# Optimization experiments

Hardware: AMD Instinct MI355X
Metric: run time of the kernel (lower is better)

The kernel has to match this reference:

```python
import jax, jax.numpy as jnp
import numpy as np

B, S, IN_F, OUT_F = 4, 2048, 4096, 4096
ALPHA = 0.01

def setup_inputs() -> dict:
    key = jax.random.key(0)
    k1, k2 = jax.random.split(key, 2)
    # int8-valued activations and weights (stored as int32 per harness dtype)
    x = jax.random.randint(k1, (B, S, IN_F), -127, 127, dtype=jnp.int32)
    weight = jax.random.randint(k2, (IN_F, OUT_F), -127, 127, dtype=jnp.int32)
    bias = jnp.zeros((1, OUT_F), dtype=jnp.float16)
    alpha = jnp.full((1,), ALPHA, dtype=jnp.float32)
    return {"x": x, "weight": weight, "bias": bias, "alpha": alpha}

def reference(x, weight, bias, alpha):
    # Faithful to forward's default (non-hybrid) path:
    # y = F.linear(x.float(), weight.t().float(), bias.float()) * alpha
    # F.linear(x, W^T) == x @ W, with W shape (in_features, out_features).
    x_shape = x.shape
    xf = x.reshape(-1, x_shape[-1]).astype(jnp.float32)          # [B*S, in]
    wf = weight.astype(jnp.float32)                               # [in, out]
    y = (xf @ wf + bias.astype(jnp.float32)) * alpha              # [B*S, out]
    return y.reshape(*x_shape[:-1], -1)                           # [B, S, out]
```

## Files before the change

### kernel.cpp

```cpp
#include <hip/hip_runtime.h>
#include <hip/hip_fp16.h>

using i32x4  = __attribute__((ext_vector_type(4)))  int;
using i32x16 = __attribute__((ext_vector_type(16))) int;

static constexpr int M  = 4 * 2048;
static constexpr int N  = 4096;
static constexpr int K  = 4096;
static constexpr int BM = 128, BN = 128, BK = 64;
static constexpr int NT = K / BK;
static constexpr int TILE = BM * BK;

static constexpr int PX_BLOCKS = (int)((size_t)M * K / 16 / 256);
static constexpr int PW_BLOCKS = (int)((size_t)N * K / 16 / 256);

__device__ __forceinline__ unsigned pack4(i32x4 v) {
  return (unsigned)((v.x & 255) | ((v.y & 255) << 8) | ((v.z & 255) << 16) | (v.w << 24));
}

__global__ __launch_bounds__(256) void pack_kernel(const int* __restrict__ x,
                                                   const int* __restrict__ w,
                                                   unsigned char* __restrict__ wa,
                                                   unsigned char* __restrict__ wb) {
  if (blockIdx.x < PX_BLOCKS) {
    unsigned g = blockIdx.x * 256 + threadIdx.x;
    unsigned tile = g >> 9, gt = g & 511;
    unsigned kg = gt >> 7, row = gt & 127;
    unsigned br = tile >> 6, kt = tile & 63;
    const int* src = x + ((size_t)(br * 128 + row) * K + kt * 64 + kg * 16);
    i32x4 v0 = *(const i32x4*)(src + 0);
    i32x4 v1 = *(const i32x4*)(src + 4);
    i32x4 v2 = *(const i32x4*)(src + 8);
    i32x4 v3 = *(const i32x4*)(src + 12);
    i32x4 d;
    d.x = (int)pack4(v0); d.y = (int)pack4(v1); d.z = (int)pack4(v2); d.w = (int)pack4(v3);
    *(i32x4*)(wa + (size_t)g * 16) = d;
  } else {
    unsigned g = (blockIdx.x - PX_BLOCKS) * 256 + threadIdx.x;
    unsigned tile = g >> 9, gt = g & 511;
    unsigned kg = gt >> 7, col = gt & 127;
    unsigned bn = tile >> 6, kt = tile & 63;
    unsigned n  = bn * 128 + col;
    unsigned k0 = kt * 64 + kg * 16;
    const int* src = w + (size_t)k0 * N + n;
    i32x4 d;
#pragma unroll
    for (int j = 0; j < 4; ++j) {
      int b0 = src[(size_t)(j * 4 + 0) * N];
      int b1 = src[(size_t)(j * 4 + 1) * N];
      int b2 = src[(size_t)(j * 4 + 2) * N];
      int b3 = src[(size_t)(j * 4 + 3) * N];
      d[j] = (b0 & 255) | ((b1 & 255) << 8) | ((b2 & 255) << 16) | (b3 << 24);
    }
    *(i32x4*)(wb + (size_t)g * 16) = d;
  }
}


__global__ __launch_bounds__(256) void gemm_i8(const unsigned char* __restrict__ wa,
                                               const unsigned char* __restrict__ wb,
                                               const __half* __restrict__ bias,
                                               const float* __restrict__ alphaP,
                                               float* __restrict__ out) {
  __shared__ __align__(16) unsigned char As[2][TILE];

  const int tid  = threadIdx.x;
  const int lane = tid & 63;
  const int w    = tid >> 6;
  const int wr   = w >> 1, wc = w & 1;
  const int l31  = lane & 31;
  const int kgl  = lane >> 5;

  const int bc = blockIdx.x;
  const int br = blockIdx.y;

  const unsigned char* ga = wa + (size_t)br * NT * TILE;
  const unsigned char* gb = wb + (size_t)bc * NT * TILE;

  const int arow = wr * 64 + l31;
  const int bcol = wc * 64 + l31;

  i32x4 p0, p1, q0, q1;
  i32x4 b[2][2][2];

#define GLOADA_P(T) do {                                             \
    const i32x4* ap = (const i32x4*)(ga + (size_t)(T) * TILE);       \
    p0 = ap[tid]; p1 = ap[tid + 256];                                \
  } while (0)

#define GLOADA_Q(T) do {                                             \
    const i32x4* ap = (const i32x4*)(ga + (size_t)(T) * TILE);       \
    q0 = ap[tid]; q1 = ap[tid + 256];                                \
  } while (0)

#define SWRITE_P(BUF) do {                                           \
    i32x4* aw = (i32x4*)&As[BUF][0];                                 \
    aw[tid] = p0; aw[tid + 256] = p1;                                \
  } while (0)

#define SWRITE_Q(BUF) do {                                           \
    i32x4* aw = (i32x4*)&As[BUF][0];                                 \
    aw[tid] = q0; aw[tid + 256] = q1;                                \
  } while (0)

#define BLOAD(PAR, T) do {                                           \
    const unsigned char* bt = gb + (size_t)(T) * TILE;               \
    b[PAR][0][0] = *(const i32x4*)(bt + (kgl    ) * 2048 + (bcol +  0) * 16); \
    b[PAR][0][1] = *(const i32x4*)(bt + (kgl    ) * 2048 + (bcol + 32) * 16); \
    b[PAR][1][0] = *(const i32x4*)(bt + (kgl + 2) * 2048 + (bcol +  0) * 16); \
    b[PAR][1][1] = *(const i32x4*)(bt + (kgl + 2) * 2048 + (bcol + 32) * 16); \
  } while (0)

  i32x16 acc[2][2] = {};

#define COMPUTE(BUF, PAR) do {                                                 \
    const unsigned char* Ab = &As[BUF][0] + kgl * 2048;                        \
    _Pragma("unroll")                                                          \
    for (int kc = 0; kc < 2; ++kc) {                                           \
      const unsigned char* Ap = Ab + kc * 4096;                                \
      i32x4 a0 = *(const i32x4*)(Ap + (arow +  0) * 16);                       \
      i32x4 a1 = *(const i32x4*)(Ap + (arow + 32) * 16);                       \
      acc[0][0] = __builtin_amdgcn_mfma_i32_32x32x32_i8(a0, b[PAR][kc][0], acc[0][0], 0, 0, 0); \
      acc[0][1] = __builtin_amdgcn_mfma_i32_32x32x32_i8(a0, b[PAR][kc][1], acc[0][1], 0, 0, 0); \
      acc[1][0] = __builtin_amdgcn_mfma_i32_32x32x32_i8(a1, b[PAR][kc][0], acc[1][0], 0, 0, 0); \
      acc[1][1] = __builtin_amdgcn_mfma_i32_32x32x32_i8(a1, b[PAR][kc][1], acc[1][1], 0, 0, 0); \
    }                                                                          \
  } while (0)

  GLOADA_P(0);
  BLOAD(0, 0);
  SWRITE_P(0);
  GLOADA_Q(1);
  BLOAD(1, 1);
  __syncthreads();

  for (int t = 0; t < NT; t += 2) {
    if (t + 2 < NT) GLOADA_P(t + 2);
    COMPUTE(0, 0);
    if (t + 2 < NT) BLOAD(0, t + 2);
    __builtin_amdgcn_sched_barrier(0);
    if (t + 1 < NT) SWRITE_Q(1);
    __syncthreads();

    if (t + 3 < NT) GLOADA_Q(t + 3);
    COMPUTE(1, 1);
    if (t + 3 < NT) BLOAD(1, t + 3);
    __builtin_amdgcn_sched_barrier(0);
    if (t + 2 < NT) SWRITE_P(0);
    __syncthreads();
  }

  const float alpha = *alphaP;
  const int row0 = br * 128 + wr * 64 + 4 * kgl;
  const int col0 = bc * 128 + wc * 64 + l31;
#pragma unroll
  for (int ni = 0; ni < 2; ++ni) {
    const int col = col0 + ni * 32;
    const float bf = __half2float(bias[col]);
#pragma unroll
    for (int mi = 0; mi < 2; ++mi) {
#pragma unroll
      for (int r = 0; r < 16; ++r) {
        const int row = row0 + mi * 32 + (r & 3) + 8 * (r >> 2);
        out[(size_t)row * N + col] = ((float)acc[mi][ni][r] + bf) * alpha;
      }
    }
  }
#undef COMPUTE
#undef GLOADA_P
#undef GLOADA_Q
#undef SWRITE_P
#undef SWRITE_Q
#undef BLOAD
}

extern "C" void kernel_launch(void* const* d_in, const int* in_sizes, int n_in,
                              void* d_out, int out_size, void* d_ws, size_t ws_size,
                              hipStream_t stream) {
  const int*    x     = (const int*)d_in[0];
  const int*    wgt   = (const int*)d_in[1];
  const __half* bias  = (const __half*)d_in[2];
  const float*  alpha = (const float*)d_in[3];
  float*        out   = (float*)d_out;

  unsigned char* wa = (unsigned char*)d_ws;
  unsigned char* wb = wa + (size_t)M * K;

  pack_kernel<<<PX_BLOCKS + PW_BLOCKS, 256, 0, stream>>>(x, wgt, wa, wb);

  dim3 grid(N / BN, M / BM);
  gemm_i8<<<grid, 256, 0, stream>>>(wa, wb, bias, alpha, out);
}
```

Baseline: 224.8 us.

## Enlarge GEMM tiles to 256x256 with 512 threads and swizzled block order

Block tiles grow from 128x128 to 256x256 with 8 waves per block, each wave computing 64x128 (2x4 MFMA accumulators). The pack layout is changed to match, the grid becomes 1D with a swizzled block-to-tile mapping, and B is prefetched directly from global memory into registers one tile ahead. The aim is higher arithmetic intensity per loaded byte and better L2 locality. In exchange, each wave uses more accumulator registers and each block needs 32KB of LDS, which may lower occupancy.

```diff
diff --git a/kernel.cpp b/kernel.cpp
--- a/kernel.cpp
+++ b/kernel.cpp
@@ -7,9 +7,10 @@
 static constexpr int M  = 4 * 2048;
 static constexpr int N  = 4096;
 static constexpr int K  = 4096;
-static constexpr int BM = 128, BN = 128, BK = 64;
+static constexpr int BM = 256, BN = 256, BK = 64;
 static constexpr int NT = K / BK;
-static constexpr int TILE = BM * BK;
+static constexpr int ATILE = BM * BK;
+static constexpr int BTILE = 128 * BK;
 
 static constexpr int PX_BLOCKS = (int)((size_t)M * K / 16 / 256);
 static constexpr int PW_BLOCKS = (int)((size_t)N * K / 16 / 256);
@@ -24,10 +25,11 @@
                                                    unsigned char* __restrict__ wb) {
   if (blockIdx.x < PX_BLOCKS) {
     unsigned g = blockIdx.x * 256 + threadIdx.x;
-    unsigned tile = g >> 9, gt = g & 511;
-    unsigned kg = gt >> 7, row = gt & 127;
-    unsigned br = tile >> 6, kt = tile & 63;
-    const int* src = x + ((size_t)(br * 128 + row) * K + kt * 64 + kg * 16);
+    unsigned row = g & 255;
+    unsigned kg  = (g >> 8) & 3;
+    unsigned kt  = (g >> 10) & 63;
+    unsigned br  = g >> 16;
+    const int* src = x + ((size_t)(br * 256 + row) * K + kt * 64 + kg * 16);
     i32x4 v0 = *(const i32x4*)(src + 0);
     i32x4 v1 = *(const i32x4*)(src + 4);
     i32x4 v2 = *(const i32x4*)(src + 8);
@@ -37,11 +39,12 @@
     *(i32x4*)(wa + (size_t)g * 16) = d;
   } else {
     unsigned g = (blockIdx.x - PX_BLOCKS) * 256 + threadIdx.x;
-    unsigned tile = g >> 9, gt = g & 511;
-    unsigned kg = gt >> 7, col = gt & 127;
-    unsigned bn = tile >> 6, kt = tile & 63;
-    unsigned n  = bn * 128 + col;
-    unsigned k0 = kt * 64 + kg * 16;
+    unsigned col = g & 127;
+    unsigned kg  = (g >> 7) & 3;
+    unsigned kt  = (g >> 9) & 63;
+    unsigned bn  = g >> 15;
+    unsigned n   = bn * 128 + col;
+    unsigned k0  = kt * 64 + kg * 16;
     const int* src = w + (size_t)k0 * N + n;
     i32x4 d;
 #pragma unroll
@@ -57,12 +60,17 @@
 }
 
 
-__global__ __launch_bounds__(256) void gemm_i8(const unsigned char* __restrict__ wa,
+#define SBAR()  do { __builtin_amdgcn_sched_barrier(0);                         \
+                     asm volatile("s_waitcnt lgkmcnt(0)" ::: "memory");         \
+                     __builtin_amdgcn_s_barrier();                              \
+                     __builtin_amdgcn_sched_barrier(0); } while (0)
+
+__global__ __launch_bounds__(512) void gemm_i8(const unsigned char* __restrict__ wa,
                                                const unsigned char* __restrict__ wb,
                                                const __half* __restrict__ bias,
                                                const float* __restrict__ alphaP,
                                                float* __restrict__ out) {
-  __shared__ __align__(16) unsigned char As[2][TILE];
+  __shared__ __align__(16) unsigned char As[2][ATILE];
 
   const int tid  = threadIdx.x;
   const int lane = tid & 63;
@@ -71,90 +79,102 @@
   const int l31  = lane & 31;
   const int kgl  = lane >> 5;
 
-  const int bc = blockIdx.x;
-  const int br = blockIdx.y;
-
-  const unsigned char* ga = wa + (size_t)br * NT * TILE;
-  const unsigned char* gb = wb + (size_t)bc * NT * TILE;
+  const int bid = blockIdx.x;
+  const int swz = (bid & 7) * 64 + (bid >> 3);
+  const int bc  = swz & 15;
+  const int br  = swz >> 4;
+
+  const unsigned char* ga  = wa + (size_t)br * NT * ATILE;
+  const unsigned char* gbp = wb + (size_t)(bc * 2 + wc) * NT * BTILE;
 
   const int arow = wr * 64 + l31;
-  const int bcol = wc * 64 + l31;
+  const int bcl  = l31;
 
   i32x4 p0, p1, q0, q1;
-  i32x4 b[2][2][2];
+  i32x4 b[2][4];
 
 #define GLOADA_P(T) do {                                             \
-    const i32x4* ap = (const i32x4*)(ga + (size_t)(T) * TILE);       \
-    p0 = ap[tid]; p1 = ap[tid + 256];                                \
+    const i32x4* ap = (const i32x4*)(ga + (size_t)(T) * ATILE);      \
+    p0 = ap[tid]; p1 = ap[tid + 512];                                \
   } while (0)
 
 #define GLOADA_Q(T) do {                                             \
-    const i32x4* ap = (const i32x4*)(ga + (size_t)(T) * TILE);       \
-    q0 = ap[tid]; q1 = ap[tid + 256];                                \
+    const i32x4* ap = (const i32x4*)(ga + (size_t)(T) * ATILE);      \
+    q0 = ap[tid]; q1 = ap[tid + 512];                                \
   } while (0)
 
 #define SWRITE_P(BUF) do {                                           \
     i32x4* aw = (i32x4*)&As[BUF][0];                                 \
-    aw[tid] = p0; aw[tid + 256] = p1;                                \
+    aw[tid] = p0; aw[tid + 512] = p1;                                \
   } while (0)
 
 #define SWRITE_Q(BUF) do {                                           \
     i32x4* aw = (i32x4*)&As[BUF][0];                                 \
-    aw[tid] = q0; aw[tid + 256] = q1;                                \
-  } while (0)
-
-#define BLOAD(PAR, T) do {                                           \
-    const unsigned char* bt = gb + (size_t)(T) * TILE;               \
-    b[PAR][0][0] = *(const i32x4*)(bt + (kgl    ) * 2048 + (bcol +  0) * 16); \
-    b[PAR][0][1] = *(const i32x4*)(bt + (kgl    ) * 2048 + (bcol + 32) * 16); \
-    b[PAR][1][0] = *(const i32x4*)(bt + (kgl + 2) * 2048 + (bcol +  0) * 16); \
-    b[PAR][1][1] = *(const i32x4*)(bt + (kgl + 2) * 2048 + (bcol + 32) * 16); \
-  } while (0)
-
-  i32x16 acc[2][2] = {};
-
-#define COMPUTE(BUF, PAR) do {                                                 \
-    const unsigned char* Ab = &As[BUF][0] + kgl * 2048;                        \
-    _Pragma("unroll")                                                          \
-    for (int kc = 0; kc < 2; ++kc) {                                           \
-      const unsigned char* Ap = Ab + kc * 4096;                                \
+    aw[tid] = q0; aw[tid + 512] = q1;                                \
+  } while (0)
+
+#define BLOAD(KC, T) do {                                            \
+    const unsigned char* bt = gbp + (size_t)(T) * BTILE + ((KC) * 2 + kgl) * 2048; \
+    b[KC][0] = *(const i32x4*)(bt + (bcl +  0) * 16);                \
+    b[KC][1] = *(const i32x4*)(bt + (bcl + 32) * 16);                \
+    b[KC][2] = *(const i32x4*)(bt + (bcl + 64) * 16);                \
+    b[KC][3] = *(const i32x4*)(bt + (bcl + 96) * 16);                \
+  } while (0)
+
+  i32x16 acc[2][4] = {};
+
+#define MFMA8(KC, A0, A1)                                                        \
+    acc[0][0] = __builtin_amdgcn_mfma_i32_32x32x32_i8(A0, b[KC][0], acc[0][0], 0,0,0); \
+    acc[0][1] = __builtin_amdgcn_mfma_i32_32x32x32_i8(A0, b[KC][1], acc[0][1], 0,0,0); \
+    acc[0][2] = __builtin_amdgcn_mfma_i32_32x32x32_i8(A0, b[KC][2], acc[0][2], 0,0,0); \
+    acc[0][3] = __builtin_amdgcn_mfma_i32_32x32x32_i8(A0, b[KC][3], acc[0][3], 0,0,0); \
+    acc[1][0] = __builtin_amdgcn_mfma_i32_32x32x32_i8(A1, b[KC][0], acc[1][0], 0,0,0); \
+    acc[1][1] = __builtin_amdgcn_mfma_i32_32x32x32_i8(A1, b[KC][1], acc[1][1], 0,0,0); \
+    acc[1][2] = __builtin_amdgcn_mfma_i32_32x32x32_i8(A1, b[KC][2], acc[1][2], 0,0,0); \
+    acc[1][3] = __builtin_amdgcn_mfma_i32_32x32x32_i8(A1, b[KC][3], acc[1][3], 0,0,0)
+
+#define STEP(T, PARITY) do {                                                   \
+    if ((T) + 2 < NT) { if (PARITY) GLOADA_Q((T) + 2); else GLOADA_P((T) + 2); } \
+    const unsigned char* Ab = &As[(T) & 1][0];                                 \
+    {                                                                 \
+      const unsigned char* Ap = Ab + kgl * 4096;                               \
       i32x4 a0 = *(const i32x4*)(Ap + (arow +  0) * 16);                       \
       i32x4 a1 = *(const i32x4*)(Ap + (arow + 32) * 16);                       \
-      acc[0][0] = __builtin_amdgcn_mfma_i32_32x32x32_i8(a0, b[PAR][kc][0], acc[0][0], 0, 0, 0); \
-      acc[0][1] = __builtin_amdgcn_mfma_i32_32x32x32_i8(a0, b[PAR][kc][1], acc[0][1], 0, 0, 0); \
-      acc[1][0] = __builtin_amdgcn_mfma_i32_32x32x32_i8(a1, b[PAR][kc][0], acc[1][0], 0, 0, 0); \
-      acc[1][1] = __builtin_amdgcn_mfma_i32_32x32x32_i8(a1, b[PAR][kc][1], acc[1][1], 0, 0, 0); \
+      MFMA8(0, a0, a1);                                                        \
+    }                                                                          \
+    if ((T) + 1 < NT) BLOAD(0, (T) + 1);        \
+    {                                                                 \
+      const unsigned char* Ap = Ab + (2 + kgl) * 4096;                         \
+      i32x4 a0 = *(const i32x4*)(Ap + (arow +  0) * 16);                       \
+      i32x4 a1 = *(const i32x4*)(Ap + (arow + 32) * 16);                       \
+      MFMA8(1, a0, a1);                                                        \
+    }                                                                          \
+    if ((T) + 1 < NT) BLOAD(1, (T) + 1);                                       \
+    __builtin_amdgcn_sched_barrier(0);                                         \
+    if ((T) + 1 < NT) {                                                        \
+             \
+      if (PARITY) SWRITE_P(((T) & 1) ^ 1); else SWRITE_Q(((T) & 1) ^ 1);       \
+      SBAR();                                                                  \
     }                                                                          \
   } while (0)
 
   GLOADA_P(0);
   BLOAD(0, 0);
+  BLOAD(1, 0);
   SWRITE_P(0);
   GLOADA_Q(1);
-  BLOAD(1, 1);
   __syncthreads();
 
   for (int t = 0; t < NT; t += 2) {
-    if (t + 2 < NT) GLOADA_P(t + 2);
-    COMPUTE(0, 0);
-    if (t + 2 < NT) BLOAD(0, t + 2);
-    __builtin_amdgcn_sched_barrier(0);
-    if (t + 1 < NT) SWRITE_Q(1);
-    __syncthreads();
-
-    if (t + 3 < NT) GLOADA_Q(t + 3);
-    COMPUTE(1, 1);
-    if (t + 3 < NT) BLOAD(1, t + 3);
-    __builtin_amdgcn_sched_barrier(0);
-    if (t + 2 < NT) SWRITE_P(0);
-    __syncthreads();
+    STEP(t, 0);
+    STEP(t + 1, 1);
   }
 
   const float alpha = *alphaP;
-  const int row0 = br * 128 + wr * 64 + 4 * kgl;
-  const int col0 = bc * 128 + wc * 64 + l31;
-#pragma unroll
-  for (int ni = 0; ni < 2; ++ni) {
+  const int row0 = br * 256 + wr * 64 + 4 * kgl;
+  const int col0 = bc * 256 + wc * 128 + l31;
+#pragma unroll
+  for (int ni = 0; ni < 4; ++ni) {
     const int col = col0 + ni * 32;
     const float bf = __half2float(bias[col]);
 #pragma unroll
@@ -166,7 +186,8 @@
       }
     }
   }
-#undef COMPUTE
+#undef STEP
+#undef MFMA8
 #undef GLOADA_P
 #undef GLOADA_Q
 #undef SWRITE_P
@@ -188,6 +209,6 @@
 
   pack_kernel<<<PX_BLOCKS + PW_BLOCKS, 256, 0, stream>>>(x, wgt, wa, wb);
 
-  dim3 grid(N / BN, M / BM);
-  gemm_i8<<<grid, 256, 0, stream>>>(wa, wb, bias, alpha, out);
-}
+  dim3 grid((M / BM) * (N / BN));
+  gemm_i8<<<grid, 512, 0, stream>>>(wa, wb, bias, alpha, out);
+}
```

New measurement: 236.8 us. +5.4%, slower.
